# Kernel tuning notes

Hardware: AMD Instinct MI355X
Metric: run time of the kernel (lower is better)

Reference implementation:

```python
import jax, jax.numpy as jnp
import numpy as np

B, N, FIN, FOUT, E = 2, 50000, 128, 64, 800000


def setup_inputs() -> dict:
    key = jax.random.key(0)
    ks = jax.random.split(key, 7)
    x = jax.random.normal(ks[0], (B, N, FIN), dtype=jnp.float32)
    W = jax.random.normal(ks[1], (FIN, FOUT), dtype=jnp.float32) * (1.0 / np.sqrt(FIN))
    W_self = jax.random.normal(ks[2], (FIN, FOUT), dtype=jnp.float32) * (1.0 / np.sqrt(FIN))
    b_self = jax.random.normal(ks[3], (FOUT,), dtype=jnp.float32) * 0.01
    edge_row = jax.random.randint(ks[4], (E,), 0, N, dtype=jnp.int32)
    edge_col = jax.random.randint(ks[5], (E,), 0, N, dtype=jnp.int32)
    edge_val = jax.random.uniform(ks[6], (E,), dtype=jnp.float32)
    return {"x": x, "W": W, "W_self": W_self, "b_self": b_self,
            "edge_row": edge_row, "edge_col": edge_col, "edge_val": edge_val}


def reference(x, W, W_self, b_self, edge_row, edge_col, edge_val):
    # x: (B, N, FIN); adjacency in COO form: out[r] += val * in[c]
    Bn, Nn, _ = x.shape
    Fo = W.shape[1]
    x_trans = jnp.einsum("bnf,fo->bno", x, W)               # (B, N, FOUT), no bias
    # Same layout trick as torch: sparse.mm over (N, B*FOUT)
    xr = x_trans.transpose(1, 0, 2).reshape(Nn, Bn * Fo)    # (N, B*FOUT)
    msgs = edge_val[:, None] * xr[edge_col]                  # (E, B*FOUT) gather
    agg = jax.ops.segment_sum(msgs, edge_row, num_segments=Nn)  # (N, B*FOUT) scatter-add
    agg = agg.reshape(Nn, Bn, Fo).transpose(1, 0, 2)         # (B, N, FOUT)
    self_c = jnp.einsum("bnf,fo->bno", x, W_self) + b_self   # Linear with bias
    return jax.nn.relu(self_c + agg)
```

## Files before the change

### kernel.cpp

```cpp
#include <hip/hip_runtime.h>
#include <hip/hip_fp16.h>

#define Bc   2
#define Nn   50000
#define FINc 128
#define FOUTc 64
#define Mtot (Bc * Nn)
#define CCOMB 128
#define GB 1563
#define CAP 64

#define NRNG   128
#define NBUCK  391
#define ABLK   256
#define RECCAP 3200
#define BCAP   2432

typedef __bf16 bf16x8 __attribute__((ext_vector_type(8)));
typedef float  f32x4  __attribute__((ext_vector_type(4)));

static __device__ inline unsigned short f2bf(float f) {
    unsigned int u = __float_as_uint(f);
    u += 0x7fffu + ((u >> 16) & 1u);
    return (unsigned short)(u >> 16);
}

__global__ __launch_bounds__(256) void prep(
    const float* __restrict__ W, const float* __restrict__ Ws,
    unsigned short* __restrict__ Bp, unsigned int* __restrict__ bfill)
{
    if (blockIdx.x < 8) {
        const int idx = blockIdx.x * 256 + threadIdx.x;
        const int lane = idx & 63;
        const int kt   = (idx >> 6) & 3;
        const int nt   = idx >> 8;
        const int n    = nt * 16 + (lane & 15);
        const int k0   = kt * 32 + (lane >> 4) * 8;
        unsigned short o8[8];
#pragma unroll
        for (int j = 0; j < 8; ++j) {
            const int f = k0 + j;
            const float v = (n < 64) ? W[f * FOUTc + n] : Ws[f * FOUTc + (n - 64)];
            o8[j] = f2bf(v);
        }
        *(uint4*)&Bp[(size_t)idx * 8] = *(uint4*)o8;
    } else {
        for (int i = threadIdx.x; i < NBUCK; i += 256) bfill[i] = 0u;
    }
}

__global__ __launch_bounds__(256) void gemm(
    const float* __restrict__ x, const unsigned short* __restrict__ Bp,
    const float* __restrict__ bself,
    unsigned short* __restrict__ xrb, float* __restrict__ outp)
{
    const int gb   = blockIdx.x;
    const int lane = threadIdx.x & 63;
    const int quad = lane >> 4;
    const int mbase = gb * 64 + (threadIdx.x >> 6) * 16;

    const int mrow   = mbase + (lane & 15);
    const int mclamp = (mrow < Mtot) ? mrow : (Mtot - 1);
    const float* __restrict__ xrow = &x[(size_t)mclamp * FINc + quad * 8];

    float4 xv[8];
#pragma unroll
    for (int kt = 0; kt < 4; ++kt) {
        xv[2 * kt]     = *(const float4*)&xrow[kt * 32];
        xv[2 * kt + 1] = *(const float4*)&xrow[kt * 32 + 4];
    }

    f32x4 acc[8] = {};

#pragma unroll
    for (int kt = 0; kt < 4; ++kt) {
        const float4 xa = xv[2 * kt];
        const float4 xb = xv[2 * kt + 1];
        bf16x8 bf;
        bf[0] = (__bf16)xa.x; bf[1] = (__bf16)xa.y;
        bf[2] = (__bf16)xa.z; bf[3] = (__bf16)xa.w;
        bf[4] = (__bf16)xb.x; bf[5] = (__bf16)xb.y;
        bf[6] = (__bf16)xb.z; bf[7] = (__bf16)xb.w;

        const bf16x8* __restrict__ abase =
            (const bf16x8*)&Bp[(size_t)(kt * 64 + lane) * 8];
#pragma unroll
        for (int nt = 0; nt < 8; ++nt) {
            const bf16x8 af = abase[nt * 4 * 64];
            acc[nt] = __builtin_amdgcn_mfma_f32_16x16x32_bf16(af, bf, acc[nt], 0, 0, 0);
        }
    }

    const int m = mbase + (lane & 15);
    if (m < Mtot) {
        const int bb = (m >= Nn) ? 1 : 0;
        const int n = m - bb * Nn;
        unsigned short* __restrict__ xp = &xrb[(size_t)n * CCOMB + bb * FOUTc];
        const int cq = quad * 4;
#pragma unroll
        for (int nt = 0; nt < 4; ++nt) {
            const int c = nt * 16 + cq;
            unsigned short h[4];
            h[0] = f2bf(acc[nt][0]); h[1] = f2bf(acc[nt][1]);
            h[2] = f2bf(acc[nt][2]); h[3] = f2bf(acc[nt][3]);
            *(uint2*)&xp[c] = *(uint2*)h;
        }
        float* __restrict__ op = &outp[(size_t)m * FOUTc];
#pragma unroll
        for (int nt = 4; nt < 8; ++nt) {
            const int o = (nt - 4) * 16 + cq;
            const float4 b4 = *(const float4*)&bself[o];
            float4 v;
            v.x = acc[nt][0] + b4.x; v.y = acc[nt][1] + b4.y;
            v.z = acc[nt][2] + b4.z; v.w = acc[nt][3] + b4.w;
            *(float4*)&op[o] = v;
        }
    }
}

__global__ __launch_bounds__(256) void bin_a(
    const int* __restrict__ erow, const int* __restrict__ ecol,
    const float* __restrict__ evalv, unsigned int* __restrict__ bfill,
    uint2* __restrict__ stage, int E, int ec)
{
    __shared__ unsigned int hist[512];
    __shared__ unsigned int incl[512];
    __shared__ unsigned int gbase[NBUCK];
    __shared__ unsigned int cur[NBUCK];
    __shared__ unsigned int recs[RECCAP * 2];

    const int tid = threadIdx.x;
    const int e0 = blockIdx.x * ec;
    int e1 = e0 + ec; if (e1 > E) e1 = E;
    if (e1 - e0 > RECCAP) e1 = e0 + RECCAP;
    const int tot = e1 - e0;

    hist[tid] = 0u; hist[tid + 256] = 0u;
    __syncthreads();

    for (int e = e0 + tid; e < e1; e += 256) {
        const int r = erow[e];
        atomicAdd(&hist[r >> 7], 1u);
    }
    __syncthreads();

    incl[tid] = hist[tid]; incl[tid + 256] = hist[tid + 256];
    __syncthreads();
    for (int off = 1; off < 512; off <<= 1) {
        const unsigned int a0 = (tid >= off) ? incl[tid - off] : 0u;
        const unsigned int a1 = ((tid + 256) >= off) ? incl[tid + 256 - off] : 0u;
        __syncthreads();
        incl[tid] += a0; incl[tid + 256] += a1;
        __syncthreads();
    }

    for (int i = tid; i < NBUCK; i += 256) {
        const unsigned int c = hist[i];
        cur[i]   = incl[i] - c;
        gbase[i] = c ? atomicAdd(&bfill[i], c) : 0u;
    }
    __syncthreads();

    for (int e = e0 + tid; e < e1; e += 256) {
        const int   r = erow[e];
        const int   c = ecol[e];
        const float v = evalv[e];
        const int  nb = r >> 7;
        const unsigned int k = atomicAdd(&cur[nb], 1u);
        recs[2 * k]     = ((unsigned int)__half_as_ushort(__float2half(v)) << 17) |
                          (unsigned int)c;
        recs[2 * k + 1] = ((unsigned int)nb << 7) | (unsigned int)(r & 127);
    }
    __syncthreads();

    for (int j = tid; j < tot; j += 256) {
        const unsigned int vc   = recs[2 * j];
        const unsigned int meta = recs[2 * j + 1];
        const int nb = (int)(meta >> 7);
        const unsigned int excl = incl[nb] - hist[nb];
        const unsigned int slot = gbase[nb] + ((unsigned int)j - excl);
        if (slot < BCAP)
            stage[(size_t)nb * BCAP + slot] = make_uint2(vc, meta);
    }
}

__global__ __launch_bounds__(256) void bin_b(
    const unsigned int* __restrict__ bfill, const uint2* __restrict__ stage,
    unsigned int* __restrict__ cvp, int* __restrict__ cntp)
{
    __shared__ unsigned int lists[NRNG * CAP];
    __shared__ unsigned int lcnt[NRNG];

    const int tid = threadIdx.x;
    const int nb  = blockIdx.x;
    const int row0 = nb << 7;
    int nrows = Nn - row0; if (nrows > NRNG) nrows = NRNG;

    for (int i = tid; i < NRNG; i += 256) lcnt[i] = 0u;
    __syncthreads();

    unsigned int cnt = bfill[nb];
    if (cnt > BCAP) cnt = BCAP;
    const uint2* __restrict__ seg = &stage[(size_t)nb * BCAP];

    for (unsigned int j = tid; j < cnt; j += 256) {
        const uint2 rec = seg[j];
        const int rl = (int)(rec.y & 127u);
        const unsigned int k = atomicAdd(&lcnt[rl], 1u);
        if (k < CAP) lists[(rl << 6) + k] = rec.x;
    }
    __syncthreads();

    unsigned int* __restrict__ dst = &cvp[(size_t)row0 << 6];
    const int words = nrows << 6;
    for (int i = tid; i < words; i += 256) dst[i] = lists[i];
    for (int rl = tid; rl < nrows; rl += 256) {
        const unsigned int c = lcnt[rl];
        cntp[(size_t)(row0 + rl) * 16] = (int)(c < CAP ? c : CAP);
    }
}

#define GATHP(W, PRED, ACC)                                                   \
    {                                                                         \
        const unsigned int w = (W);                                           \
        unsigned int col = w & 0x1FFFFu;                                      \
        col = (col < Nn) ? col : 0u;           \
        const float vv = (PRED) ? __half2float(__ushort_as_half(              \
                             (unsigned short)(w >> 17))) : 0.0f;              \
        const uint4 raw = *(const uint4*)&xrb[(size_t)col * CCOMB + c0];      \
        ACC[0] = fmaf(vv, __uint_as_float(raw.x << 16),         ACC[0]);      \
        ACC[1] = fmaf(vv, __uint_as_float(raw.x & 0xffff0000u), ACC[1]);      \
        ACC[2] = fmaf(vv, __uint_as_float(raw.y << 16),         ACC[2]);      \
        ACC[3] = fmaf(vv, __uint_as_float(raw.y & 0xffff0000u), ACC[3]);      \
        ACC[4] = fmaf(vv, __uint_as_float(raw.z << 16),         ACC[4]);      \
        ACC[5] = fmaf(vv, __uint_as_float(raw.z & 0xffff0000u), ACC[5]);      \
        ACC[6] = fmaf(vv, __uint_as_float(raw.w << 16),         ACC[6]);      \
        ACC[7] = fmaf(vv, __uint_as_float(raw.w & 0xffff0000u), ACC[7]);      \
    }

__global__ __launch_bounds__(256) void row_gather(
    const int* __restrict__ cntp, const unsigned int* __restrict__ cvp,
    const unsigned short* __restrict__ xrb, float* __restrict__ outp)
{
    const int j    = blockIdx.x;
    const int low3 = j & 7;
    const int h    = (low3 >= 4) ? 1 : 0;
    const int ord  = (j >> 3) * 4 + (low3 & 3);
    int n = ord * 4 + (threadIdx.x >> 6);
    n = __builtin_amdgcn_readfirstlane(n);

    const int lane = threadIdx.x & 63;
    const int slot = lane >> 3;
    const int c0   = h * 64 + (lane & 7) * 8;
    const unsigned int* __restrict__ seg = &cvp[(size_t)n << 6];

    const int kc = min(cntp[(size_t)n * 16], CAP);
    const unsigned int u0 = seg[slot];
    const unsigned int u1 = seg[8 + slot];

    float aA[8] = {0.f, 0.f, 0.f, 0.f, 0.f, 0.f, 0.f, 0.f};

    GATHP(u0, slot < kc,     aA);
    GATHP(u1, slot + 8 < kc, aA);

    for (int e = 16 + slot; e < kc; e += 8) {
        const unsigned int u = seg[e];
        GATHP(u, true, aA);
    }

#pragma unroll
    for (int i = 0; i < 8; ++i) {
        aA[i] += __shfl_down(aA[i], 8);
        aA[i] += __shfl_down(aA[i], 16);
        aA[i] += __shfl_down(aA[i], 32);
    }

    if (lane < 8) {
        const size_t m = (size_t)h * Nn + n;
        const int o = lane * 8;
        float* __restrict__ op = &outp[m * FOUTc + o];
        float4 s0 = *(float4*)&op[0];
        float4 s1 = *(float4*)&op[4];
        s0.x = fmaxf(s0.x + aA[0], 0.0f); s0.y = fmaxf(s0.y + aA[1], 0.0f);
        s0.z = fmaxf(s0.z + aA[2], 0.0f); s0.w = fmaxf(s0.w + aA[3], 0.0f);
        s1.x = fmaxf(s1.x + aA[4], 0.0f); s1.y = fmaxf(s1.y + aA[5], 0.0f);
        s1.z = fmaxf(s1.z + aA[6], 0.0f); s1.w = fmaxf(s1.w + aA[7], 0.0f);
        *(float4*)&op[0] = s0;
        *(float4*)&op[4] = s1;
    }
}

extern "C" void kernel_launch(void* const* d_in, const int* in_sizes, int n_in,
                              void* d_out, int out_size, void* d_ws, size_t ws_size,
                              hipStream_t stream)
{
    const float* x    = (const float*)d_in[0];
    const float* W    = (const float*)d_in[1];
    const float* Ws   = (const float*)d_in[2];
    const float* bs   = (const float*)d_in[3];
    const int*   erow = (const int*)d_in[4];
    const int*   ecol = (const int*)d_in[5];
    const float* eval = (const float*)d_in[6];
    float* outp = (float*)d_out;
    const int E = in_sizes[4];

    unsigned short* xrb = (unsigned short*)d_ws;
    unsigned int*   cvp = (unsigned int*)(xrb + (size_t)Nn * CCOMB);
    int*            cntp = (int*)(cvp + ((size_t)Nn << 6));
    unsigned short* Bp  = (unsigned short*)(cntp + (size_t)Nn * 16);
    unsigned int*   bfill = (unsigned int*)(Bp + 16384);
    uint2*          stage = (uint2*)(bfill + 512);

    const int ec = (E + ABLK - 1) / ABLK;

    prep<<<9, 256, 0, stream>>>(W, Ws, Bp, bfill);

    gemm<<<GB, 256, 0, stream>>>(x, Bp, bs, xrb, outp);

    bin_a<<<ABLK, 256, 0, stream>>>(erow, ecol, eval, bfill, stage, E, ec);
    bin_b<<<NBUCK, 256, 0, stream>>>(bfill, stage, cvp, cntp);

    row_gather<<<Nn / 2, 256, 0, stream>>>(cntp, cvp, xrb, outp);
}
```

Measured before the change: 185.3 us.

## Fuse edge binning into GEMM launch via interleaved block roles

```diff
diff --git a/kernel.cpp b/kernel.cpp
--- a/kernel.cpp
+++ b/kernel.cpp
@@ -13,8 +13,8 @@
 #define NRNG   128
 #define NBUCK  391
 #define ABLK   256
-#define RECCAP 3200
 #define BCAP   2432
+#define FUSED_GRID (ABLK * 9)
 
 typedef __bf16 bf16x8 __attribute__((ext_vector_type(8)));
 typedef float  f32x4  __attribute__((ext_vector_type(4)));
@@ -49,12 +49,58 @@
     }
 }
 
-__global__ __launch_bounds__(256) void gemm(
+__global__ __launch_bounds__(256) void gemm_bina(
     const float* __restrict__ x, const unsigned short* __restrict__ Bp,
     const float* __restrict__ bself,
-    unsigned short* __restrict__ xrb, float* __restrict__ outp)
-{
-    const int gb   = blockIdx.x;
+    unsigned short* __restrict__ xrb, float* __restrict__ outp,
+    const int* __restrict__ erow, const int* __restrict__ ecol,
+    const float* __restrict__ evalv, unsigned int* __restrict__ bfill,
+    uint2* __restrict__ stage, int E, int ec)
+{
+    const int b  = blockIdx.x;
+    const int r9 = b % 9;
+
+    if (r9 == 8) {
+        __shared__ unsigned int hist[512];
+        __shared__ unsigned int gbase[NBUCK];
+        __shared__ unsigned int cur[NBUCK];
+
+        const int tid = threadIdx.x;
+        const int ord = b / 9;
+        const int e0 = ord * ec;
+        int e1 = e0 + ec; if (e1 > E) e1 = E;
+
+        hist[tid] = 0u; hist[tid + 256] = 0u;
+        for (int i = tid; i < NBUCK; i += 256) cur[i] = 0u;
+        __syncthreads();
+
+        for (int e = e0 + tid; e < e1; e += 256)
+            atomicAdd(&hist[erow[e] >> 7], 1u);
+        __syncthreads();
+
+        for (int i = tid; i < NBUCK; i += 256) {
+            const unsigned int c = hist[i];
+            gbase[i] = c ? atomicAdd(&bfill[i], c) : 0u;
+        }
+        __syncthreads();
+
+        for (int e = e0 + tid; e < e1; e += 256) {
+            const int   r = erow[e];
+            const int   c = ecol[e];
+            const float v = evalv[e];
+            const int  nb = r >> 7;
+            const unsigned int k = gbase[nb] + atomicAdd(&cur[nb], 1u);
+            if (k < BCAP)
+                stage[(size_t)nb * BCAP + k] = make_uint2(
+                    ((unsigned int)__half_as_ushort(__float2half(v)) << 17) |
+                        (unsigned int)c,
+                    (unsigned int)(r & 127));
+        }
+        return;
+    }
+
+    const int gb = b - (b + 1) / 9;
+    if (gb >= GB) return;
     const int lane = threadIdx.x & 63;
     const int quad = lane >> 4;
     const int mbase = gb * 64 + (threadIdx.x >> 6) * 16;
@@ -115,72 +161,6 @@
             v.z = acc[nt][2] + b4.z; v.w = acc[nt][3] + b4.w;
             *(float4*)&op[o] = v;
         }
-    }
-}
-
-__global__ __launch_bounds__(256) void bin_a(
-    const int* __restrict__ erow, const int* __restrict__ ecol,
-    const float* __restrict__ evalv, unsigned int* __restrict__ bfill,
-    uint2* __restrict__ stage, int E, int ec)
-{
-    __shared__ unsigned int hist[512];
-    __shared__ unsigned int incl[512];
-    __shared__ unsigned int gbase[NBUCK];
-    __shared__ unsigned int cur[NBUCK];
-    __shared__ unsigned int recs[RECCAP * 2];
-
-    const int tid = threadIdx.x;
-    const int e0 = blockIdx.x * ec;
-    int e1 = e0 + ec; if (e1 > E) e1 = E;
-    if (e1 - e0 > RECCAP) e1 = e0 + RECCAP;
-    const int tot = e1 - e0;
-
-    hist[tid] = 0u; hist[tid + 256] = 0u;
-    __syncthreads();
-
-    for (int e = e0 + tid; e < e1; e += 256) {
-        const int r = erow[e];
-        atomicAdd(&hist[r >> 7], 1u);
-    }
-    __syncthreads();
-
-    incl[tid] = hist[tid]; incl[tid + 256] = hist[tid + 256];
-    __syncthreads();
-    for (int off = 1; off < 512; off <<= 1) {
-        const unsigned int a0 = (tid >= off) ? incl[tid - off] : 0u;
-        const unsigned int a1 = ((tid + 256) >= off) ? incl[tid + 256 - off] : 0u;
-        __syncthreads();
-        incl[tid] += a0; incl[tid + 256] += a1;
-        __syncthreads();
-    }
-
-    for (int i = tid; i < NBUCK; i += 256) {
-        const unsigned int c = hist[i];
-        cur[i]   = incl[i] - c;
-        gbase[i] = c ? atomicAdd(&bfill[i], c) : 0u;
-    }
-    __syncthreads();
-
-    for (int e = e0 + tid; e < e1; e += 256) {
-        const int   r = erow[e];
-        const int   c = ecol[e];
-        const float v = evalv[e];
-        const int  nb = r >> 7;
-        const unsigned int k = atomicAdd(&cur[nb], 1u);
-        recs[2 * k]     = ((unsigned int)__half_as_ushort(__float2half(v)) << 17) |
-                          (unsigned int)c;
-        recs[2 * k + 1] = ((unsigned int)nb << 7) | (unsigned int)(r & 127);
-    }
-    __syncthreads();
-
-    for (int j = tid; j < tot; j += 256) {
-        const unsigned int vc   = recs[2 * j];
-        const unsigned int meta = recs[2 * j + 1];
-        const int nb = (int)(meta >> 7);
-        const unsigned int excl = incl[nb] - hist[nb];
-        const unsigned int slot = gbase[nb] + ((unsigned int)j - excl);
-        if (slot < BCAP)
-            stage[(size_t)nb * BCAP + slot] = make_uint2(vc, meta);
     }
 }
 
@@ -315,9 +295,10 @@
 
     prep<<<9, 256, 0, stream>>>(W, Ws, Bp, bfill);
 
-    gemm<<<GB, 256, 0, stream>>>(x, Bp, bs, xrb, outp);
-
-    bin_a<<<ABLK, 256, 0, stream>>>(erow, ecol, eval, bfill, stage, E, ec);
+    gemm_bina<<<FUSED_GRID, 256, 0, stream>>>(x, Bp, bs, xrb, outp,
+                                              erow, ecol, eval, bfill,
+                                              stage, E, ec);
+
     bin_b<<<NBUCK, 256, 0, stream>>>(bfill, stage, cvp, cntp);
 
     row_gather<<<Nn / 2, 256, 0, stream>>>(cntp, cvp, xrb, outp);
```

Measured after the change: 179.1 us. 3.3% less time.
